# Kernel tuning notes

Hardware: AMD Instinct MI355X
Metric: run time of the kernel (lower is better)

Reference implementation:

```python
import jax, jax.numpy as jnp
import numpy as np

B, S, E, H, D = 4, 2048, 1024, 16, 64


def setup_inputs() -> dict:
    key = jax.random.key(0)
    ks = jax.random.split(key, 6)
    scale_in = 1.0 / np.sqrt(E)
    return {
        "x": jax.random.normal(ks[0], (B, S, E), dtype=jnp.float32),
        "Wq": jax.random.normal(ks[1], (H, E, D), dtype=jnp.float32) * scale_in,
        "bq": jnp.zeros((H, D), dtype=jnp.float32),
        "Wk": jax.random.normal(ks[2], (H, E, D), dtype=jnp.float32) * scale_in,
        "bk": jnp.zeros((H, D), dtype=jnp.float32),
        "Wv": jax.random.normal(ks[3], (H, E, D), dtype=jnp.float32) * scale_in,
        "bv": jnp.zeros((H, D), dtype=jnp.float32),
        "Wo": jax.random.normal(ks[4], (H * D, E), dtype=jnp.float32) * (1.0 / np.sqrt(H * D)),
        "bo": jnp.zeros((E,), dtype=jnp.float32),
    }


def reference(x, Wq, bq, Wk, bk, Wv, bv, Wo, bo):
    # Per-head Q/K/V projections, batched over heads: [B,S,E] x [H,E,D] -> [B,H,S,D]
    q = jnp.einsum("bse,hed->bhsd", x, Wq) + bq[None, :, None, :]
    k = jnp.einsum("bse,hed->bhsd", x, Wk) + bk[None, :, None, :]
    v = jnp.einsum("bse,hed->bhsd", x, Wv) + bv[None, :, None, :]

    d = q.shape[-1]
    scores = jnp.einsum("bhqd,bhkd->bhqk", q, k) / jnp.sqrt(jnp.asarray(d, q.dtype))
    # Causal mask (registered tril buffer of size max_seq_len in HeadAttention)
    seq = scores.shape[-1]
    causal = jnp.tril(jnp.ones((seq, seq), dtype=bool))
    scores = jnp.where(causal[None, None, :, :], scores, jnp.asarray(-1e9, scores.dtype))
    attn = jax.nn.softmax(scores, axis=-1)
    out = jnp.einsum("bhqk,bhkd->bhqd", attn, v)  # [B,H,S,D]

    # Concat heads: [B,S,H*D], then output projection (dropout is identity in eval)
    out = out.transpose(0, 2, 1, 3).reshape(out.shape[0], out.shape[2], -1)
    return out @ Wo + bo
```

## Files before the change

kernel.cpp:

```cpp
#include <hip/hip_runtime.h>

typedef __bf16 bf16x8 __attribute__((ext_vector_type(8)));
typedef __bf16 bf16x4 __attribute__((ext_vector_type(4)));
typedef float  f32x4  __attribute__((ext_vector_type(4)));

#define B_    4
#define S_    2048
#define E_    1024
#define H_    16
#define D_    64
#define MROWS (B_*S_)
#define HD3   3072

#define SCORE_SCALE 0.18033688011112043f

__device__ __forceinline__ void load_lds16(const void* g, void* l) {
  __builtin_amdgcn_global_load_lds((__attribute__((address_space(1))) void*)g,
                                   (__attribute__((address_space(3))) void*)l,
                                   16, 0, 0);
}

__device__ __forceinline__ f32x4 mfma16(bf16x8 a, bf16x8 b, f32x4 c) {
  return __builtin_amdgcn_mfma_f32_16x16x32_bf16(a, b, c, 0, 0, 0);
}

__device__ __forceinline__ int swz(int row, int dchunk) {
  return row * 64 + ((dchunk ^ (row & 7)) * 8);
}


__global__ void prep(const float4* __restrict__ x, const float* __restrict__ Wq,
                     const float* __restrict__ Wk, const float* __restrict__ Wv,
                     const float* __restrict__ bq, const float* __restrict__ bk,
                     const float* __restrict__ bv, const float* __restrict__ Wo,
                     __bf16* __restrict__ xb, __bf16* __restrict__ Wt,
                     float* __restrict__ bqkv, __bf16* __restrict__ Wot) {
  __shared__ float t[64][65];
  int bid = blockIdx.x;
  if (bid < 8192) {
    int id = bid * 256 + threadIdx.x;
    float4 v = x[id];
    bf16x4 o = { (__bf16)v.x, (__bf16)v.y, (__bf16)v.z, (__bf16)v.w };
    *(bf16x4*)(xb + 4 * (size_t)id) = o;
    return;
  }
  int tx = threadIdx.x & 63;
  int ty = threadIdx.x >> 6;
  if (bid < 8960) {
    int b2 = bid - 8192;
    int e0 = (b2 & 15) * 64;
    int h  = (b2 >> 4) & 15;
    int p  = b2 >> 8;
    const float* W    = (p == 0) ? Wq : (p == 1) ? Wk : Wv;
    const float* bsrc = (p == 0) ? bq : (p == 1) ? bk : bv;
#pragma unroll
    for (int r = 0; r < 16; ++r) {
      int eL = ty + r * 4;
      t[eL][tx] = W[((size_t)h * 1024 + (e0 + eL)) * 64 + tx];
    }
    __syncthreads();
#pragma unroll
    for (int r = 0; r < 16; ++r) {
      int d = ty + r * 4;
      Wt[((size_t)(p * 1024 + h * 64 + d)) * 1024 + e0 + tx] = (__bf16)t[tx][d];
    }
    if ((b2 & 15) == 0 && threadIdx.x < 64)
      bqkv[p * 1024 + h * 64 + threadIdx.x] = bsrc[h * 64 + threadIdx.x];
  } else {
    int b2 = bid - 8960;
    int hd0 = (b2 >> 4) * 64;
    int e0  = (b2 & 15) * 64;
#pragma unroll
    for (int r = 0; r < 16; ++r) {
      int hdL = ty + r * 4;
      t[hdL][tx] = Wo[(size_t)(hd0 + hdL) * 1024 + e0 + tx];
    }
    __syncthreads();
#pragma unroll
    for (int r = 0; r < 16; ++r) {
      int eL = ty + r * 4;
      Wot[(size_t)(e0 + eL) * 1024 + hd0 + tx] = (__bf16)t[tx][eL];
    }
  }
}


template <int MODE>
__global__ __launch_bounds__(256) void gemm_bt(const __bf16* __restrict__ A,
                                               const __bf16* __restrict__ Bt,
                                               const float* __restrict__ bias,
                                               void* __restrict__ Cout,
                                               __bf16* __restrict__ VT,
                                               int M, int N, int K) {
  __shared__ __attribute__((aligned(16))) __bf16 As[128 * 64];
  __shared__ __attribute__((aligned(16))) __bf16 Bs[128 * 64];
  int tid = threadIdx.x, wave = tid >> 6, lane = tid & 63;
  int quad = lane >> 4, cc = lane & 15;
  int nb = N >> 7;
  int bm = (int)blockIdx.x / nb, bn = (int)blockIdx.x % nb;
  const __bf16* Abase = A + (size_t)bm * 128 * K;
  const __bf16* Bbase = Bt + (size_t)bn * 128 * K;
  int wr = (wave >> 1) * 64, wc = (wave & 1) * 64;
  f32x4 acc[4][4];
#pragma unroll
  for (int i = 0; i < 4; ++i)
#pragma unroll
    for (int j = 0; j < 4; ++j) acc[i][j] = (f32x4){0.f, 0.f, 0.f, 0.f};

  int srow[4], scol[4];
#pragma unroll
  for (int p = 0; p < 4; ++p) {
    int g = tid + p * 256;
    srow[p] = g >> 3;
    scol[p] = ((g & 7) ^ (srow[p] & 7)) * 8;
  }
#pragma unroll
  for (int p = 0; p < 4; ++p) {
    load_lds16(Abase + (size_t)srow[p] * K + scol[p], &As[(tid + p * 256) * 8]);
    load_lds16(Bbase + (size_t)srow[p] * K + scol[p], &Bs[(tid + p * 256) * 8]);
  }

  for (int k0 = 0; k0 < K; k0 += 64) {
    __syncthreads();
    bf16x8 af[2][4], bf[2][4];
#pragma unroll
    for (int kk = 0; kk < 2; ++kk) {
#pragma unroll
      for (int i = 0; i < 4; ++i) af[kk][i] = *(const bf16x8*)&As[swz(wr + i * 16 + cc, kk * 4 + quad)];
#pragma unroll
      for (int j = 0; j < 4; ++j) bf[kk][j] = *(const bf16x8*)&Bs[swz(wc + j * 16 + cc, kk * 4 + quad)];
    }
    __syncthreads();
    if (k0 + 64 < K) {
      int kn = k0 + 64;
#pragma unroll
      for (int p = 0; p < 4; ++p) {
        load_lds16(Abase + (size_t)srow[p] * K + kn + scol[p], &As[(tid + p * 256) * 8]);
        load_lds16(Bbase + (size_t)srow[p] * K + kn + scol[p], &Bs[(tid + p * 256) * 8]);
      }
    }
#pragma unroll
    for (int kk = 0; kk < 2; ++kk)
#pragma unroll
      for (int i = 0; i < 4; ++i)
#pragma unroll
        for (int j = 0; j < 4; ++j) acc[kk ? i : i][j] = mfma16(af[kk][i], bf[kk][j], acc[i][j]);
  }

#pragma unroll
  for (int j = 0; j < 4; ++j) {
    int col = bn * 128 + wc + j * 16 + cc;
    float bv = bias[col];
#pragma unroll
    for (int i = 0; i < 4; ++i) {
      int row0 = bm * 128 + wr + i * 16 + quad * 4;
      if (MODE == 0) {
#pragma unroll
        for (int r = 0; r < 4; ++r)
          ((float*)Cout)[(size_t)(row0 + r) * N + col] = acc[i][j][r] + bv;
      } else if (col < 2048) {
        float sc = (col < 1024) ? SCORE_SCALE : 1.0f;
#pragma unroll
        for (int r = 0; r < 4; ++r)
          ((__bf16*)Cout)[(size_t)(row0 + r) * 2048 + col] = (__bf16)((acc[i][j][r] + bv) * sc);
      } else {
        int bh = (row0 >> 11) * 16 + ((col >> 6) & 15);
        int d  = col & 63;
        bf16x4 pk;
#pragma unroll
        for (int r = 0; r < 4; ++r) pk[r] = (__bf16)(acc[i][j][r] + bv);
        *(bf16x4*)&VT[((size_t)(bh * 64 + d)) * 2048 + (row0 & 2047)] = pk;
      }
    }
  }
}


__global__ __launch_bounds__(512, 4) void attn(const __bf16* __restrict__ QKb,
                                               const __bf16* __restrict__ VT,
                                               __bf16* __restrict__ O) {
  int bx = blockIdx.x;
  int bh = bx & 63;
  int qt = (bx < 256) ? (7 - (bx >> 6)) : ((bx >> 6) - 4);
  int h  = bh & 15;
  int b  = bh >> 4;
  int q0 = qt * 256;
  int tid = threadIdx.x, wave = tid >> 6, lane = tid & 63;
  int quad = lane >> 4, c = lane & 15;

  __shared__ __attribute__((aligned(16))) __bf16 smem[32768];
  __bf16* Qs = smem;
  __bf16* Ks = smem + 16384;
  __bf16* Vs = smem + 24576;
  __bf16* Ps = smem + wave * 2048;

  const __bf16* Qbase = QKb + (size_t)(b * S_ + q0) * 2048 + h * 64;
  const __bf16* Vbase = VT + (size_t)bh * (64 * 2048);
#pragma unroll
  for (int p = 0; p < 4; ++p) {
    int g = tid + p * 512;
    int row = g >> 3, pch = g & 7;
    load_lds16(Qbase + (size_t)row * 2048 + (pch ^ (row & 7)) * 8, &Qs[g * 8]);
  }
  {
    const __bf16* Kb = QKb + (size_t)(b * S_) * 2048 + 1024 + h * 64;
    int row = tid >> 3, pch = tid & 7;
    load_lds16(Kb + (size_t)row * 2048 + (pch ^ (row & 7)) * 8, &Ks[tid * 8]);
    load_lds16(Vbase + (size_t)row * 2048 + (pch ^ (row & 7)) * 8, &Vs[tid * 8]);
  }
  __syncthreads();

  bf16x8 qf[2][2];
#pragma unroll
  for (int i = 0; i < 2; ++i)
#pragma unroll
    for (int kk = 0; kk < 2; ++kk)
      qf[i][kk] = *(const bf16x8*)&Qs[swz(wave * 32 + i * 16 + c, kk * 4 + quad)];

  const __bf16 one_b = (__bf16)1.0f;
  bf16x8 ones = { one_b, one_b, one_b, one_b, one_b, one_b, one_b, one_b };

  f32x4 acc_o[2][4], acc_l[2];
#pragma unroll
  for (int i = 0; i < 2; ++i) {
    acc_l[i] = (f32x4){0.f, 0.f, 0.f, 0.f};
#pragma unroll
    for (int j = 0; j < 4; ++j) acc_o[i][j] = (f32x4){0.f, 0.f, 0.f, 0.f};
  }

  int qwave = q0 + wave * 32;
  int ntiles = qt * 4 + 4;
  for (int t = 0; t < ntiles; ++t) {
    int cur = t & 1;
    if (t + 1 < ntiles) {
      int kv1 = (t + 1) * 64;
      const __bf16* Kb = QKb + (size_t)(b * S_ + kv1) * 2048 + 1024 + h * 64;
      const __bf16* Vb = Vbase + kv1;
      int row = tid >> 3, pch = tid & 7;
      load_lds16(Kb + (size_t)row * 2048 + (pch ^ (row & 7)) * 8,
                 &Ks[(cur ^ 1) * 4096 + tid * 8]);
      load_lds16(Vb + (size_t)row * 2048 + (pch ^ (row & 7)) * 8,
                 &Vs[(cur ^ 1) * 4096 + tid * 8]);
    }

    int kv0 = t * 64;
    if (kv0 <= qwave + 31) {
      const __bf16* Kc = Ks + cur * 4096;
      const __bf16* Vc = Vs + cur * 4096;

      f32x4 acc_t[2][4];
#pragma unroll
      for (int i = 0; i < 2; ++i)
#pragma unroll
        for (int j = 0; j < 4; ++j) acc_t[i][j] = (f32x4){0.f, 0.f, 0.f, 0.f};
      bf16x8 kf[4][2];
#pragma unroll
      for (int j = 0; j < 4; ++j)
#pragma unroll
        for (int kk = 0; kk < 2; ++kk)
          kf[j][kk] = *(const bf16x8*)&Kc[swz(j * 16 + c, kk * 4 + quad)];
#pragma unroll
      for (int i = 0; i < 2; ++i)
#pragma unroll
        for (int j = 0; j < 4; ++j)
#pragma unroll
          for (int kk = 0; kk < 2; ++kk)
            acc_t[i][j] = mfma16(kf[j][kk], qf[i][kk], acc_t[i][j]);

      bool domask = (kv0 + 63 > qwave);
#pragma unroll
      for (int i = 0; i < 2; ++i) {
        int q_l = i * 16 + c;
        int q_g = qwave + q_l;
#pragma unroll
        for (int j = 0; j < 4; ++j) {
          bf16x4 pk;
#pragma unroll
          for (int r = 0; r < 4; ++r) {
            float p = __builtin_amdgcn_exp2f(acc_t[i][j][r]);
            if (domask) {
              int kv = kv0 + j * 16 + quad * 4 + r;
              p = (kv > q_g) ? 0.f : p;
            }
            pk[r] = (__bf16)p;
          }
          int dch8 = j * 2 + (quad >> 1);
          int phys = q_l * 64 + ((dch8 ^ (q_l & 7)) * 8) + (quad & 1) * 4;
          *(bf16x4*)&Ps[phys] = pk;
        }
      }

      bf16x8 pf[2][2], vf[4][2];
#pragma unroll
      for (int i = 0; i < 2; ++i)
#pragma unroll
        for (int kk = 0; kk < 2; ++kk)
          pf[i][kk] = *(const bf16x8*)&Ps[swz(i * 16 + c, kk * 4 + quad)];
#pragma unroll
      for (int j = 0; j < 4; ++j)
#pragma unroll
        for (int kk = 0; kk < 2; ++kk)
          vf[j][kk] = *(const bf16x8*)&Vc[swz(j * 16 + c, kk * 4 + quad)];
#pragma unroll
      for (int i = 0; i < 2; ++i) {
#pragma unroll
        for (int j = 0; j < 4; ++j)
#pragma unroll
          for (int kk = 0; kk < 2; ++kk)
            acc_o[i][j] = mfma16(pf[i][kk], vf[j][kk], acc_o[i][j]);
        acc_l[i] = mfma16(pf[i][0], ones, acc_l[i]);
        acc_l[i] = mfma16(pf[i][1], ones, acc_l[i]);
      }
    }

    __syncthreads();
  }

  __bf16* Obase = O + (size_t)(b * S_ + q0) * 1024 + h * 64;
#pragma unroll
  for (int i = 0; i < 2; ++i)
#pragma unroll
    for (int r = 0; r < 4; ++r) {
      float rl = 1.0f / acc_l[i][r];
      int row = wave * 32 + i * 16 + quad * 4 + r;
#pragma unroll
      for (int j = 0; j < 4; ++j)
        Obase[(size_t)row * 1024 + j * 16 + c] = (__bf16)(acc_o[i][j][r] * rl);
    }
}


extern "C" void kernel_launch(void* const* d_in, const int* in_sizes, int n_in,
                              void* d_out, int out_size, void* d_ws, size_t ws_size,
                              hipStream_t stream) {
  (void)in_sizes; (void)n_in; (void)out_size; (void)ws_size;
  const float* x  = (const float*)d_in[0];
  const float* Wq = (const float*)d_in[1];
  const float* bq = (const float*)d_in[2];
  const float* Wk = (const float*)d_in[3];
  const float* bk = (const float*)d_in[4];
  const float* Wv = (const float*)d_in[5];
  const float* bv = (const float*)d_in[6];
  const float* Wo = (const float*)d_in[7];
  const float* bo = (const float*)d_in[8];

  char* w = (char*)d_ws;
  __bf16* xb   = (__bf16*)(w);
  __bf16* Wt   = (__bf16*)(w + (16ull << 20));
  __bf16* Wot  = (__bf16*)(w + (22ull << 20));
  float*  bqkv = (float*) (w + (24ull << 20));
  __bf16* QKb  = (__bf16*)(w + (25ull << 20));
  __bf16* Ob   = (__bf16*)(w + (57ull << 20));
  __bf16* VT   = (__bf16*)(w + (73ull << 20));

  prep   <<<9216, 256, 0, stream>>>((const float4*)x, Wq, Wk, Wv, bq, bk, bv, Wo,
                                    xb, Wt, bqkv, Wot);
  gemm_bt<1><<<dim3((MROWS / 128) * (3072 / 128)), 256, 0, stream>>>(xb, Wt, bqkv, (void*)QKb, VT, MROWS, 3072, 1024);
  attn   <<<512, 512, 0, stream>>>(QKb, VT, Ob);
  gemm_bt<0><<<dim3((MROWS / 128) * (1024 / 128)), 256, 0, stream>>>(Ob, Wot, bo, d_out, nullptr, MROWS, 1024, 1024);
}
```

Baseline: 242.4 us.

## Halve attention query tile, remap GEMM blocks per XCD, add MFMA priority

```diff
diff --git a/kernel.cpp b/kernel.cpp
--- a/kernel.cpp
+++ b/kernel.cpp
@@ -97,7 +97,10 @@
   int tid = threadIdx.x, wave = tid >> 6, lane = tid & 63;
   int quad = lane >> 4, cc = lane & 15;
   int nb = N >> 7;
-  int bm = (int)blockIdx.x / nb, bn = (int)blockIdx.x % nb;
+  int nwg = (int)gridDim.x;
+  int bid = (int)blockIdx.x;
+  bid = (bid & 7) * (nwg >> 3) + (bid >> 3);
+  int bm = bid / nb, bn = bid % nb;
   const __bf16* Abase = A + (size_t)bm * 128 * K;
   const __bf16* Bbase = Bt + (size_t)bn * 128 * K;
   int wr = (wave >> 1) * 64, wc = (wave & 1) * 64;
@@ -144,7 +147,7 @@
 #pragma unroll
       for (int i = 0; i < 4; ++i)
 #pragma unroll
-        for (int j = 0; j < 4; ++j) acc[kk ? i : i][j] = mfma16(af[kk][i], bf[kk][j], acc[i][j]);
+        for (int j = 0; j < 4; ++j) acc[i][j] = mfma16(af[kk][i], bf[kk][j], acc[i][j]);
   }
 
 #pragma unroll
@@ -176,37 +179,42 @@
 }
 
 
-__global__ __launch_bounds__(512, 4) void attn(const __bf16* __restrict__ QKb,
+__global__ __launch_bounds__(256, 3) void attn(const __bf16* __restrict__ QKb,
                                                const __bf16* __restrict__ VT,
                                                __bf16* __restrict__ O) {
   int bx = blockIdx.x;
   int bh = bx & 63;
-  int qt = (bx < 256) ? (7 - (bx >> 6)) : ((bx >> 6) - 4);
+  int g  = bx >> 6;
+  int qt = (g < 8) ? (15 - g) : (g - 8);
   int h  = bh & 15;
   int b  = bh >> 4;
-  int q0 = qt * 256;
+  int q0 = qt * 128;
   int tid = threadIdx.x, wave = tid >> 6, lane = tid & 63;
   int quad = lane >> 4, c = lane & 15;
 
-  __shared__ __attribute__((aligned(16))) __bf16 smem[32768];
+  __shared__ __attribute__((aligned(16))) __bf16 smem[24576];
   __bf16* Qs = smem;
-  __bf16* Ks = smem + 16384;
-  __bf16* Vs = smem + 24576;
+  __bf16* Ks = smem + 8192;
+  __bf16* Vs = smem + 16384;
   __bf16* Ps = smem + wave * 2048;
 
   const __bf16* Qbase = QKb + (size_t)(b * S_ + q0) * 2048 + h * 64;
   const __bf16* Vbase = VT + (size_t)bh * (64 * 2048);
 #pragma unroll
   for (int p = 0; p < 4; ++p) {
-    int g = tid + p * 512;
-    int row = g >> 3, pch = g & 7;
-    load_lds16(Qbase + (size_t)row * 2048 + (pch ^ (row & 7)) * 8, &Qs[g * 8]);
+    int gi = tid + p * 256;
+    int row = gi >> 3, pch = gi & 7;
+    load_lds16(Qbase + (size_t)row * 2048 + (pch ^ (row & 7)) * 8, &Qs[gi * 8]);
   }
   {
     const __bf16* Kb = QKb + (size_t)(b * S_) * 2048 + 1024 + h * 64;
-    int row = tid >> 3, pch = tid & 7;
-    load_lds16(Kb + (size_t)row * 2048 + (pch ^ (row & 7)) * 8, &Ks[tid * 8]);
-    load_lds16(Vbase + (size_t)row * 2048 + (pch ^ (row & 7)) * 8, &Vs[tid * 8]);
+#pragma unroll
+    for (int p = 0; p < 2; ++p) {
+      int gi = tid + p * 256;
+      int row = gi >> 3, pch = gi & 7;
+      load_lds16(Kb + (size_t)row * 2048 + (pch ^ (row & 7)) * 8, &Ks[gi * 8]);
+      load_lds16(Vbase + (size_t)row * 2048 + (pch ^ (row & 7)) * 8, &Vs[gi * 8]);
+    }
   }
   __syncthreads();
 
@@ -229,18 +237,22 @@
   }
 
   int qwave = q0 + wave * 32;
-  int ntiles = qt * 4 + 4;
+  int ntiles = qt * 2 + 2;
   for (int t = 0; t < ntiles; ++t) {
     int cur = t & 1;
     if (t + 1 < ntiles) {
       int kv1 = (t + 1) * 64;
       const __bf16* Kb = QKb + (size_t)(b * S_ + kv1) * 2048 + 1024 + h * 64;
       const __bf16* Vb = Vbase + kv1;
-      int row = tid >> 3, pch = tid & 7;
-      load_lds16(Kb + (size_t)row * 2048 + (pch ^ (row & 7)) * 8,
-                 &Ks[(cur ^ 1) * 4096 + tid * 8]);
-      load_lds16(Vb + (size_t)row * 2048 + (pch ^ (row & 7)) * 8,
-                 &Vs[(cur ^ 1) * 4096 + tid * 8]);
+#pragma unroll
+      for (int p = 0; p < 2; ++p) {
+        int gi = tid + p * 256;
+        int row = gi >> 3, pch = gi & 7;
+        load_lds16(Kb + (size_t)row * 2048 + (pch ^ (row & 7)) * 8,
+                   &Ks[(cur ^ 1) * 4096 + gi * 8]);
+        load_lds16(Vb + (size_t)row * 2048 + (pch ^ (row & 7)) * 8,
+                   &Vs[(cur ^ 1) * 4096 + gi * 8]);
+      }
     }
 
     int kv0 = t * 64;
@@ -259,6 +271,7 @@
 #pragma unroll
         for (int kk = 0; kk < 2; ++kk)
           kf[j][kk] = *(const bf16x8*)&Kc[swz(j * 16 + c, kk * 4 + quad)];
+      __builtin_amdgcn_s_setprio(1);
 #pragma unroll
       for (int i = 0; i < 2; ++i)
 #pragma unroll
@@ -266,6 +279,7 @@
 #pragma unroll
           for (int kk = 0; kk < 2; ++kk)
             acc_t[i][j] = mfma16(kf[j][kk], qf[i][kk], acc_t[i][j]);
+      __builtin_amdgcn_s_setprio(0);
 
       bool domask = (kv0 + 63 > qwave);
 #pragma unroll
@@ -301,6 +315,7 @@
 #pragma unroll
         for (int kk = 0; kk < 2; ++kk)
           vf[j][kk] = *(const bf16x8*)&Vc[swz(j * 16 + c, kk * 4 + quad)];
+      __builtin_amdgcn_s_setprio(1);
 #pragma unroll
       for (int i = 0; i < 2; ++i) {
 #pragma unroll
@@ -311,6 +326,7 @@
         acc_l[i] = mfma16(pf[i][0], ones, acc_l[i]);
         acc_l[i] = mfma16(pf[i][1], ones, acc_l[i]);
       }
+      __builtin_amdgcn_s_setprio(0);
     }
 
     __syncthreads();
@@ -356,6 +372,6 @@
   prep   <<<9216, 256, 0, stream>>>((const float4*)x, Wq, Wk, Wv, bq, bk, bv, Wo,
                                     xb, Wt, bqkv, Wot);
   gemm_bt<1><<<dim3((MROWS / 128) * (3072 / 128)), 256, 0, stream>>>(xb, Wt, bqkv, (void*)QKb, VT, MROWS, 3072, 1024);
-  attn   <<<512, 512, 0, stream>>>(QKb, VT, Ob);
+  attn   <<<1024, 256, 0, stream>>>(QKb, VT, Ob);
   gemm_bt<0><<<dim3((MROWS / 128) * (1024 / 128)), 256, 0, stream>>>(Ob, Wot, bo, d_out, nullptr, MROWS, 1024, 1024);
 }
```

New measurement: 245.5 us. No clear change (+1.3%).
